# Kernel optimization log

Measured on AMD Instinct MI355X. Metric: run time of the kernel, lower is better.

## Reference

```python
import jax, jax.numpy as jnp
import numpy as np
from jax import lax

B, N, T, E = 16, 2048, 48, 32
C0, C1 = 64, 64
H1, H2 = 256, 128
NPRED = 12
KT = 3
SCALE = float(np.sqrt(C1))


def setup_inputs() -> dict:
    key = jax.random.key(0)
    ks = jax.random.split(key, 20)
    def lin(k, fin, fout):
        bound = 1.0 / np.sqrt(fin)
        kw, kb = jax.random.split(k)
        W = jax.random.uniform(kw, (fin, fout), jnp.float32, -bound, bound)
        b = jax.random.uniform(kb, (fout,), jnp.float32, -bound, bound)
        return W, b
    x = jax.random.normal(ks[0], (B, N, T, E), jnp.float32)
    W_in, b_in = lin(ks[1], E, C0)
    # conv kernel laid out WIO for lax.conv_general_dilated ('NWC','WIO','NWC')
    bound = 1.0 / np.sqrt(C0 * KT)
    W_conv = jax.random.uniform(ks[2], (KT, C0, C1), jnp.float32, -bound, bound)
    b_conv = jax.random.uniform(ks[3], (C1,), jnp.float32, -bound, bound)
    Wq, bq = lin(ks[4], C1, C1)
    Wk, bk = lin(ks[5], C1, C1)
    Wv, bv = lin(ks[6], C1, C1)
    W1, b1 = lin(ks[7], C1, H1)
    W2, b2 = lin(ks[8], H1, H2)
    W3, b3 = lin(ks[9], H2, NPRED)
    return dict(x=x, W_in=W_in, b_in=b_in, W_conv=W_conv, b_conv=b_conv,
                Wq=Wq, bq=bq, Wk=Wk, bk=bk, Wv=Wv, bv=bv,
                W1=W1, b1=b1, W2=W2, b2=b2, W3=W3, b3=b3)


def reference(x, W_in, b_in, W_conv, b_conv, Wq, bq, Wk, bk, Wv, bv,
              W1, b1, W2, b2, W3, b3):
    Bs, Ns, Ts, Es = x.shape
    # input linear, fold nodes into batch (weights shared across nodes)
    h = jnp.einsum('bnte,ec->bntc', x, W_in) + b_in          # [B,N,T,C0]
    h = h.reshape(Bs * Ns, Ts, C0)                            # [BN,T,C0]
    # temporal conv over T, kernel KT, pad 1 each side (matches Conv2d (Kt,1), pad (1,0))
    h = lax.conv_general_dilated(h, W_conv, window_strides=(1,),
                                 padding=[(1, 1)],
                                 dimension_numbers=('NWC', 'WIO', 'NWC')) + b_conv
    h = jax.nn.relu(h)                                        # [BN,T,C1]
    q = h @ Wq + bq
    k = h @ Wk + bk
    v = h @ Wv + bv
    scores = jnp.einsum('btd,bsd->bts', q, k) / SCALE         # [BN,T,T]
    attn = jax.nn.softmax(scores, axis=-1)
    ctx = jnp.einsum('bts,bsd->btd', attn, v)                 # [BN,T,C1]
    last = ctx[:, -1, :]                                      # [BN,C1]
    # output MLP (dropout is identity in eval/reference)
    z = jax.nn.relu(last @ W1 + b1)
    z = jax.nn.relu(z @ W2 + b2)
    pred = z @ W3 + b3                                        # [BN,NPRED]
    out = pred.reshape(Bs, Ns, NPRED)                         # [B,N,P]
    out = jnp.transpose(out, (0, 2, 1))[:, None]              # [B,1,P,N]
    return out
```

## Files before the change

kernel.cpp:

```cpp
#include <hip/hip_runtime.h>
#include <math.h>

#define TT 48
#define NSEQ (16*2048)
#define NP 12

typedef __bf16 bf16x8 __attribute__((ext_vector_type(8)));
typedef float  f32x4  __attribute__((ext_vector_type(4)));

#define OFF_WCC 0
#define OFF_WK  6144
#define OFF_WV  10240
#define OFF_WQ  14336
#define OFF_W1  18432
#define OFF_W2  34816
#define WS_BTOT 33792
#define WS_BC0  33856
#define WS_BC2  33920
#define WS_CTX  33984

__device__ __forceinline__ f32x4 zero4() {
  f32x4 z; z[0] = 0.f; z[1] = 0.f; z[2] = 0.f; z[3] = 0.f; return z;
}

__global__ __launch_bounds__(256) void prep_kernel(
    const float* __restrict__ W_in, const float* __restrict__ b_in,
    const float* __restrict__ W_conv, const float* __restrict__ b_conv,
    const float* __restrict__ Wk, const float* __restrict__ Wv,
    const float* __restrict__ Wq, const float* __restrict__ W1,
    const float* __restrict__ W2, float* __restrict__ ws)
{
  __bf16* wsb = (__bf16*)ws;
  const int tid = threadIdx.x;
  const int bid = blockIdx.x;
  if (bid < 24) {
    int gid = bid * 256 + tid;
    int kk = gid >> 6;
    int c  = gid & 63;
    int dt = kk >> 5;
    int e  = kk & 31;
    const float* wrow = W_in + e * 64;
    const float* wc   = W_conv + dt * 4096 + c;
    float acc = 0.f;
    #pragma unroll 8
    for (int c0 = 0; c0 < 64; ++c0)
      acc = fmaf(wrow[c0], wc[c0 * 64], acc);
    wsb[OFF_WCC + ((kk >> 3) * 64 + c) * 8 + (kk & 7)] = (__bf16)acc;
  } else if (bid < 40) {
    int gid = (bid - 24) * 256 + tid;
    int kk = gid >> 6, c = gid & 63;
    wsb[OFF_WK + ((kk >> 3) * 64 + c) * 8 + (kk & 7)] = (__bf16)Wk[kk * 64 + c];
  } else if (bid < 56) {
    int gid = (bid - 40) * 256 + tid;
    int kk = gid >> 6, c = gid & 63;
    wsb[OFF_WV + ((kk >> 3) * 64 + c) * 8 + (kk & 7)] = (__bf16)Wv[kk * 64 + c];
  } else if (bid < 72) {
    int gid = (bid - 56) * 256 + tid;
    int kk = gid >> 6, c = gid & 63;
    wsb[OFF_WQ + ((kk >> 3) * 64 + c) * 8 + (kk & 7)] = (__bf16)Wq[kk * 64 + c];
  } else if (bid < 136) {
    int gid = (bid - 72) * 256 + tid;
    int kk = gid >> 8, n = gid & 255;
    wsb[OFF_W1 + ((kk >> 3) * 256 + n) * 8 + (kk & 7)] = (__bf16)W1[kk * 256 + n];
  } else if (bid < 264) {
    int gid = (bid - 136) * 256 + tid;
    int kk = gid >> 7, n = gid & 127;
    wsb[OFF_W2 + ((kk >> 3) * 128 + n) * 8 + (kk & 7)] = (__bf16)W2[kk * 128 + n];
  } else if (tid < 64) {
    int c = tid;
    float s[3];
    for (int dt = 0; dt < 3; ++dt) {
      const float* wc = W_conv + dt * 4096 + c;
      float a = 0.f;
      for (int c0 = 0; c0 < 64; ++c0) a = fmaf(b_in[c0], wc[c0 * 64], a);
      s[dt] = a;
    }
    ws[WS_BC0 + c]  = s[0];
    ws[WS_BC2 + c]  = s[2];
    ws[WS_BTOT + c] = s[0] + s[1] + s[2] + b_conv[c];
  }
}

__global__ __launch_bounds__(256, 2) void attn_kernel(
    const float* __restrict__ x,
    const float* __restrict__ bq, const float* __restrict__ bk,
    const float* __restrict__ bv,
    const float* __restrict__ ws, float* __restrict__ ctx)
{
  __shared__ __bf16 h1s[4][48 * 66];

  const int tid  = threadIdx.x;
  const int lane = tid & 63;
  const int wv   = tid >> 6;
  const int m16  = lane & 15;
  const int quad = lane >> 4;
  const int seq  = blockIdx.x * 4 + wv;
  __bf16* h1 = h1s[wv];

  const __bf16* wsb  = (const __bf16*)ws;
  const bf16x8* WccB = (const bf16x8*)(wsb + OFF_WCC);
  const bf16x8* WkB  = (const bf16x8*)(wsb + OFF_WK);
  const bf16x8* WvB  = (const bf16x8*)(wsb + OFF_WV);
  const bf16x8* WqB  = (const bf16x8*)(wsb + OFF_WQ);
  const float*  wsf  = ws;
  const float*  xseq = x + (size_t)seq * (TT * 32);

  f32x4 cacc[3][4];
  #pragma unroll
  for (int mt = 0; mt < 3; ++mt)
    #pragma unroll
    for (int nt = 0; nt < 4; ++nt) cacc[mt][nt] = zero4();

  #pragma unroll
  for (int ks = 0; ks < 3; ++ks) {
    bf16x8 bf[4];
    #pragma unroll
    for (int nt = 0; nt < 4; ++nt)
      bf[nt] = WccB[(ks * 4 + quad) * 64 + nt * 16 + m16];
    #pragma unroll
    for (int mt = 0; mt < 3; ++mt) {
      const int tg = mt * 16 + m16 + ks - 1;
      const bool need_guard = (mt == 0 && ks == 0) || (mt == 2 && ks == 2);
      bf16x8 af;
      if (!need_guard || (tg >= 0 && tg < 48)) {
        const float* ap = xseq + tg * 32 + quad * 8;
        float4 a0 = *(const float4*)ap;
        float4 a1 = *(const float4*)(ap + 4);
        af[0] = (__bf16)a0.x; af[1] = (__bf16)a0.y;
        af[2] = (__bf16)a0.z; af[3] = (__bf16)a0.w;
        af[4] = (__bf16)a1.x; af[5] = (__bf16)a1.y;
        af[6] = (__bf16)a1.z; af[7] = (__bf16)a1.w;
      } else {
        #pragma unroll
        for (int j = 0; j < 8; ++j) af[j] = (__bf16)0.f;
      }
      #pragma unroll
      for (int nt = 0; nt < 4; ++nt)
        cacc[mt][nt] = __builtin_amdgcn_mfma_f32_16x16x32_bf16(af, bf[nt], cacc[mt][nt], 0, 0, 0);
    }
  }

  #pragma unroll
  for (int nt = 0; nt < 4; ++nt) {
    const int c = nt * 16 + m16;
    const float bt = wsf[WS_BTOT + c];
    const float b0 = wsf[WS_BC0 + c];
    const float b2 = wsf[WS_BC2 + c];
    #pragma unroll
    for (int mt = 0; mt < 3; ++mt)
      #pragma unroll
      for (int r = 0; r < 4; ++r) {
        const int trow = mt * 16 + quad * 4 + r;
        float v = cacc[mt][nt][r] + bt;
        if (mt == 0 && r == 0 && quad == 0) v -= b0;
        if (mt == 2 && r == 3 && quad == 3) v -= b2;
        h1[trow * 66 + c] = (__bf16)fmaxf(v, 0.f);
      }
  }
  __asm__ __volatile__("s_waitcnt lgkmcnt(0)" ::: "memory");

  bf16x8 a8[3][2];
  #pragma unroll
  for (int mt = 0; mt < 3; ++mt)
    #pragma unroll
    for (int ks = 0; ks < 2; ++ks)
      a8[mt][ks] = *(const bf16x8*)&h1[(mt * 16 + m16) * 66 + ks * 32 + quad * 8];

  float qvv[4];
  {
    f32x4 qa[4] = {zero4(), zero4(), zero4(), zero4()};
    #pragma unroll
    for (int ks = 0; ks < 2; ++ks)
      #pragma unroll
      for (int nt = 0; nt < 4; ++nt)
        qa[nt] = __builtin_amdgcn_mfma_f32_16x16x32_bf16(
            a8[2][ks], WqB[(ks * 4 + quad) * 64 + nt * 16 + m16], qa[nt], 0, 0, 0);
    #pragma unroll
    for (int nt = 0; nt < 4; ++nt) {
      float q47 = __shfl(qa[nt][3], m16 + 48, 64);
      qvv[nt] = (q47 + bq[nt * 16 + m16]) * 0.125f;
    }
  }

  float p[3][4];
  {
    f32x4 ka[3][4];
    #pragma unroll
    for (int mt = 0; mt < 3; ++mt)
      #pragma unroll
      for (int nt = 0; nt < 4; ++nt) ka[mt][nt] = zero4();
    #pragma unroll
    for (int ks = 0; ks < 2; ++ks) {
      bf16x8 bf[4];
      #pragma unroll
      for (int nt = 0; nt < 4; ++nt)
        bf[nt] = WkB[(ks * 4 + quad) * 64 + nt * 16 + m16];
      #pragma unroll
      for (int mt = 0; mt < 3; ++mt)
        #pragma unroll
        for (int nt = 0; nt < 4; ++nt)
          ka[mt][nt] = __builtin_amdgcn_mfma_f32_16x16x32_bf16(a8[mt][ks], bf[nt], ka[mt][nt], 0, 0, 0);
    }
    float qb = 0.f;
    #pragma unroll
    for (int nt = 0; nt < 4; ++nt) qb = fmaf(qvv[nt], bk[nt * 16 + m16], qb);
    float s[3][4];
    #pragma unroll
    for (int mt = 0; mt < 3; ++mt)
      #pragma unroll
      for (int r = 0; r < 4; ++r) {
        float t = qb;
        #pragma unroll
        for (int nt = 0; nt < 4; ++nt) t = fmaf(qvv[nt], ka[mt][nt][r], t);
        t += __shfl_xor(t, 1, 64);
        t += __shfl_xor(t, 2, 64);
        t += __shfl_xor(t, 4, 64);
        t += __shfl_xor(t, 8, 64);
        s[mt][r] = t;
      }
    float mx = -INFINITY;
    #pragma unroll
    for (int mt = 0; mt < 3; ++mt)
      #pragma unroll
      for (int r = 0; r < 4; ++r) mx = fmaxf(mx, s[mt][r]);
    mx = fmaxf(mx, __shfl_xor(mx, 16, 64));
    mx = fmaxf(mx, __shfl_xor(mx, 32, 64));
    float l = 0.f;
    #pragma unroll
    for (int mt = 0; mt < 3; ++mt)
      #pragma unroll
      for (int r = 0; r < 4; ++r) {
        float e = __expf(s[mt][r] - mx);
        p[mt][r] = e;
        l += e;
      }
    l += __shfl_xor(l, 16, 64);
    l += __shfl_xor(l, 32, 64);
    float rl = 1.f / l;
    #pragma unroll
    for (int mt = 0; mt < 3; ++mt)
      #pragma unroll
      for (int r = 0; r < 4; ++r) p[mt][r] *= rl;
  }

  {
    f32x4 va[3][4];
    #pragma unroll
    for (int mt = 0; mt < 3; ++mt)
      #pragma unroll
      for (int nt = 0; nt < 4; ++nt) va[mt][nt] = zero4();
    #pragma unroll
    for (int ks = 0; ks < 2; ++ks) {
      bf16x8 bf[4];
      #pragma unroll
      for (int nt = 0; nt < 4; ++nt)
        bf[nt] = WvB[(ks * 4 + quad) * 64 + nt * 16 + m16];
      #pragma unroll
      for (int mt = 0; mt < 3; ++mt)
        #pragma unroll
        for (int nt = 0; nt < 4; ++nt)
          va[mt][nt] = __builtin_amdgcn_mfma_f32_16x16x32_bf16(a8[mt][ks], bf[nt], va[mt][nt], 0, 0, 0);
    }
    float cx[4] = {0.f, 0.f, 0.f, 0.f};
    #pragma unroll
    for (int nt = 0; nt < 4; ++nt)
      #pragma unroll
      for (int mt = 0; mt < 3; ++mt)
        #pragma unroll
        for (int r = 0; r < 4; ++r)
          cx[nt] = fmaf(p[mt][r], va[mt][nt][r], cx[nt]);
    #pragma unroll
    for (int nt = 0; nt < 4; ++nt) {
      cx[nt] += __shfl_xor(cx[nt], 16, 64);
      cx[nt] += __shfl_xor(cx[nt], 32, 64);
    }
    if (quad == 0) {
      #pragma unroll
      for (int nt = 0; nt < 4; ++nt)
        ctx[(size_t)seq * 64 + nt * 16 + m16] = cx[nt] + bv[nt * 16 + m16];
    }
  }
}

__global__ __launch_bounds__(256) void mlp_kernel(
    const float* __restrict__ ctx, const float* __restrict__ ws,
    const float* __restrict__ b1, const float* __restrict__ b2,
    const float* __restrict__ W3, const float* __restrict__ b3,
    float* __restrict__ out)
{
  __shared__ __bf16 Xs[16 * 68];
  __shared__ __bf16 z1[16 * 264];
  __shared__ float  z2[16 * 132];

  const int tid  = threadIdx.x;
  const int r0   = blockIdx.x * 16;
  const int lane = tid & 63;
  const int wv   = tid >> 6;
  const int m16  = lane & 15;
  const int quad = lane >> 4;

  const __bf16* wsb = (const __bf16*)ws;
  const bf16x8* W1B = (const bf16x8*)(wsb + OFF_W1);
  const bf16x8* W2B = (const bf16x8*)(wsb + OFF_W2);

  {
    int row = tid >> 4, c4 = (tid & 15) * 4;
    float4 a = *(const float4*)(ctx + (size_t)(r0 + row) * 64 + c4);
    __bf16* d = &Xs[row * 68 + c4];
    d[0] = (__bf16)a.x; d[1] = (__bf16)a.y; d[2] = (__bf16)a.z; d[3] = (__bf16)a.w;
  }
  __syncthreads();

  {
    bf16x8 a8[2];
    #pragma unroll
    for (int ks = 0; ks < 2; ++ks)
      a8[ks] = *(const bf16x8*)&Xs[m16 * 68 + ks * 32 + quad * 8];
    f32x4 acc[4] = {zero4(), zero4(), zero4(), zero4()};
    #pragma unroll
    for (int nt = 0; nt < 4; ++nt) {
      int n = wv * 64 + nt * 16 + m16;
      #pragma unroll
      for (int ks = 0; ks < 2; ++ks)
        acc[nt] = __builtin_amdgcn_mfma_f32_16x16x32_bf16(
            a8[ks], W1B[(ks * 4 + quad) * 256 + n], acc[nt], 0, 0, 0);
    }
    #pragma unroll
    for (int nt = 0; nt < 4; ++nt) {
      int n = wv * 64 + nt * 16 + m16;
      float bb = b1[n];
      #pragma unroll
      for (int r = 0; r < 4; ++r)
        z1[(quad * 4 + r) * 264 + n] = (__bf16)fmaxf(acc[nt][r] + bb, 0.f);
    }
  }
  __syncthreads();

  {
    f32x4 acc[2] = {zero4(), zero4()};
    #pragma unroll 2
    for (int ks = 0; ks < 8; ++ks) {
      bf16x8 a = *(const bf16x8*)&z1[m16 * 264 + ks * 32 + quad * 8];
      #pragma unroll
      for (int nt = 0; nt < 2; ++nt)
        acc[nt] = __builtin_amdgcn_mfma_f32_16x16x32_bf16(
            a, W2B[(ks * 4 + quad) * 128 + wv * 32 + nt * 16 + m16], acc[nt], 0, 0, 0);
    }
    #pragma unroll
    for (int nt = 0; nt < 2; ++nt) {
      int n = wv * 32 + nt * 16 + m16;
      float bb = b2[n];
      #pragma unroll
      for (int r = 0; r < 4; ++r)
        z2[(quad * 4 + r) * 132 + n] = fmaxf(acc[nt][r] + bb, 0.f);
    }
  }
  __syncthreads();

  if (tid < 16 * NP) {
    int r = tid / NP, pp = tid - r * NP;
    const float* zr = z2 + r * 132;
    float a0 = b3[pp], a1 = 0.f, a2 = 0.f, a3 = 0.f;
    #pragma unroll 8
    for (int k = 0; k < 128; k += 4) {
      float4 f = *(const float4*)(zr + k);
      a0 = fmaf(f.x, W3[k * NP + pp],       a0);
      a1 = fmaf(f.y, W3[(k + 1) * NP + pp], a1);
      a2 = fmaf(f.z, W3[(k + 2) * NP + pp], a2);
      a3 = fmaf(f.w, W3[(k + 3) * NP + pp], a3);
    }
    float a = (a0 + a1) + (a2 + a3);
    int row = r0 + r;
    int bb = row >> 11, nn = row & 2047;
    out[(size_t)bb * (NP * 2048) + pp * 2048 + nn] = a;
  }
}

extern "C" void kernel_launch(void* const* d_in, const int* in_sizes, int n_in,
                              void* d_out, int out_size, void* d_ws, size_t ws_size,
                              hipStream_t stream) {
  const float* x      = (const float*)d_in[0];
  const float* W_in   = (const float*)d_in[1];
  const float* b_in   = (const float*)d_in[2];
  const float* W_conv = (const float*)d_in[3];
  const float* b_conv = (const float*)d_in[4];
  const float* Wq     = (const float*)d_in[5];
  const float* bq     = (const float*)d_in[6];
  const float* Wk     = (const float*)d_in[7];
  const float* bk     = (const float*)d_in[8];
  const float* Wv     = (const float*)d_in[9];
  const float* bv     = (const float*)d_in[10];
  const float* W1     = (const float*)d_in[11];
  const float* b1     = (const float*)d_in[12];
  const float* W2     = (const float*)d_in[13];
  const float* b2     = (const float*)d_in[14];
  const float* W3     = (const float*)d_in[15];
  const float* b3     = (const float*)d_in[16];
  float* ws  = (float*)d_ws;
  float* out = (float*)d_out;

  prep_kernel<<<265, 256, 0, stream>>>(W_in, b_in, W_conv, b_conv, Wk, Wv, Wq, W1, W2, ws);
  attn_kernel<<<NSEQ / 4, 256, 0, stream>>>(x, bq, bk, bv, ws, ws + WS_CTX);
  mlp_kernel<<<NSEQ / 16, 256, 0, stream>>>(ws + WS_CTX, ws, b1, b2, W3, b3, out);
}
```

Before: 399.1 us.

## Split attention MFMA accumulators into column halves and shrink blocks for occupancy

The attention kernel now computes the conv, K and V projections in two 32-column halves, so only 6 accumulator tiles are live at once instead of 12. The conv input fragments are loaded into registers up front, and the fp32-to-bf16 conversion uses packed bf162 conversions. Blocks drop to 128 threads (2 waves, 2 sequences each) with launch bounds of 4 blocks per CU, aiming for lower register pressure and higher occupancy. The cost is reloading weight fragments per half and holding 9 preloaded input fragments, which could offset the register savings.

```diff
diff --git a/kernel.cpp b/kernel.cpp
--- a/kernel.cpp
+++ b/kernel.cpp
@@ -1,4 +1,5 @@
 #include <hip/hip_runtime.h>
+#include <hip/hip_bf16.h>
 #include <math.h>
 
 #define TT 48
@@ -21,6 +22,17 @@
 
 __device__ __forceinline__ f32x4 zero4() {
   f32x4 z; z[0] = 0.f; z[1] = 0.f; z[2] = 0.f; z[3] = 0.f; return z;
+}
+
+union PackU { bf16x8 v; __hip_bfloat162 h[4]; };
+
+__device__ __forceinline__ bf16x8 pack8(float4 a, float4 b) {
+  PackU u;
+  u.h[0] = __float22bfloat162_rn(make_float2(a.x, a.y));
+  u.h[1] = __float22bfloat162_rn(make_float2(a.z, a.w));
+  u.h[2] = __float22bfloat162_rn(make_float2(b.x, b.y));
+  u.h[3] = __float22bfloat162_rn(make_float2(b.z, b.w));
+  return u.v;
 }
 
 __global__ __launch_bounds__(256) void prep_kernel(
@@ -81,20 +93,20 @@
   }
 }
 
-__global__ __launch_bounds__(256, 2) void attn_kernel(
+__global__ __launch_bounds__(128, 4) void attn_kernel(
     const float* __restrict__ x,
     const float* __restrict__ bq, const float* __restrict__ bk,
     const float* __restrict__ bv,
     const float* __restrict__ ws, float* __restrict__ ctx)
 {
-  __shared__ __bf16 h1s[4][48 * 66];
+  __shared__ __bf16 h1s[2][48 * 66];
 
   const int tid  = threadIdx.x;
   const int lane = tid & 63;
   const int wv   = tid >> 6;
   const int m16  = lane & 15;
   const int quad = lane >> 4;
-  const int seq  = blockIdx.x * 4 + wv;
+  const int seq  = blockIdx.x * 2 + wv;
   __bf16* h1 = h1s[wv];
 
   const __bf16* wsb  = (const __bf16*)ws;
@@ -105,57 +117,54 @@
   const float*  wsf  = ws;
   const float*  xseq = x + (size_t)seq * (TT * 32);
 
-  f32x4 cacc[3][4];
+  bf16x8 af[3][3];
   #pragma unroll
   for (int mt = 0; mt < 3; ++mt)
     #pragma unroll
-    for (int nt = 0; nt < 4; ++nt) cacc[mt][nt] = zero4();
-
-  #pragma unroll
-  for (int ks = 0; ks < 3; ++ks) {
-    bf16x8 bf[4];
-    #pragma unroll
-    for (int nt = 0; nt < 4; ++nt)
-      bf[nt] = WccB[(ks * 4 + quad) * 64 + nt * 16 + m16];
-    #pragma unroll
-    for (int mt = 0; mt < 3; ++mt) {
+    for (int ks = 0; ks < 3; ++ks) {
       const int tg = mt * 16 + m16 + ks - 1;
       const bool need_guard = (mt == 0 && ks == 0) || (mt == 2 && ks == 2);
-      bf16x8 af;
       if (!need_guard || (tg >= 0 && tg < 48)) {
         const float* ap = xseq + tg * 32 + quad * 8;
-        float4 a0 = *(const float4*)ap;
-        float4 a1 = *(const float4*)(ap + 4);
-        af[0] = (__bf16)a0.x; af[1] = (__bf16)a0.y;
-        af[2] = (__bf16)a0.z; af[3] = (__bf16)a0.w;
-        af[4] = (__bf16)a1.x; af[5] = (__bf16)a1.y;
-        af[6] = (__bf16)a1.z; af[7] = (__bf16)a1.w;
+        af[mt][ks] = pack8(*(const float4*)ap, *(const float4*)(ap + 4));
       } else {
         #pragma unroll
-        for (int j = 0; j < 8; ++j) af[j] = (__bf16)0.f;
-      }
-      #pragma unroll
-      for (int nt = 0; nt < 4; ++nt)
-        cacc[mt][nt] = __builtin_amdgcn_mfma_f32_16x16x32_bf16(af, bf[nt], cacc[mt][nt], 0, 0, 0);
-    }
-  }
+        for (int j = 0; j < 8; ++j) af[mt][ks][j] = (__bf16)0.f;
+      }
+    }
 
   #pragma unroll
-  for (int nt = 0; nt < 4; ++nt) {
-    const int c = nt * 16 + m16;
-    const float bt = wsf[WS_BTOT + c];
-    const float b0 = wsf[WS_BC0 + c];
-    const float b2 = wsf[WS_BC2 + c];
-    #pragma unroll
-    for (int mt = 0; mt < 3; ++mt)
-      #pragma unroll
-      for (int r = 0; r < 4; ++r) {
-        const int trow = mt * 16 + quad * 4 + r;
-        float v = cacc[mt][nt][r] + bt;
-        if (mt == 0 && r == 0 && quad == 0) v -= b0;
-        if (mt == 2 && r == 3 && quad == 3) v -= b2;
-        h1[trow * 66 + c] = (__bf16)fmaxf(v, 0.f);
-      }
+  for (int nh = 0; nh < 2; ++nh) {
+    f32x4 acc[3][2];
+    #pragma unroll
+    for (int mt = 0; mt < 3; ++mt) { acc[mt][0] = zero4(); acc[mt][1] = zero4(); }
+    #pragma unroll
+    for (int ks = 0; ks < 3; ++ks) {
+      bf16x8 b0 = WccB[(ks * 4 + quad) * 64 + nh * 32 + m16];
+      bf16x8 b1 = WccB[(ks * 4 + quad) * 64 + nh * 32 + 16 + m16];
+      #pragma unroll
+      for (int mt = 0; mt < 3; ++mt) {
+        acc[mt][0] = __builtin_amdgcn_mfma_f32_16x16x32_bf16(af[mt][ks], b0, acc[mt][0], 0, 0, 0);
+        acc[mt][1] = __builtin_amdgcn_mfma_f32_16x16x32_bf16(af[mt][ks], b1, acc[mt][1], 0, 0, 0);
+      }
+    }
+    #pragma unroll
+    for (int j = 0; j < 2; ++j) {
+      const int c = nh * 32 + j * 16 + m16;
+      const float bt = wsf[WS_BTOT + c];
+      const float b0v = wsf[WS_BC0 + c];
+      const float b2v = wsf[WS_BC2 + c];
+      #pragma unroll
+      for (int mt = 0; mt < 3; ++mt)
+        #pragma unroll
+        for (int r = 0; r < 4; ++r) {
+          const int trow = mt * 16 + quad * 4 + r;
+          float v = acc[mt][j][r] + bt;
+          if (mt == 0 && r == 0 && quad == 0) v -= b0v;
+          if (mt == 2 && r == 3 && quad == 3) v -= b2v;
+          h1[trow * 66 + c] = (__bf16)fmaxf(v, 0.f);
+        }
+    }
   }
   __asm__ __volatile__("s_waitcnt lgkmcnt(0)" ::: "memory");
 
@@ -184,34 +193,44 @@
 
   float p[3][4];
   {
-    f32x4 ka[3][4];
+    float s[3][4];
+    {
+      float qb = 0.f;
+      #pragma unroll
+      for (int nt = 0; nt < 4; ++nt) qb = fmaf(qvv[nt], bk[nt * 16 + m16], qb);
+      #pragma unroll
+      for (int mt = 0; mt < 3; ++mt)
+        #pragma unroll
+        for (int r = 0; r < 4; ++r) s[mt][r] = qb;
+    }
+    #pragma unroll
+    for (int nh = 0; nh < 2; ++nh) {
+      f32x4 ka[3][2];
+      #pragma unroll
+      for (int mt = 0; mt < 3; ++mt) { ka[mt][0] = zero4(); ka[mt][1] = zero4(); }
+      #pragma unroll
+      for (int ks = 0; ks < 2; ++ks) {
+        bf16x8 b0 = WkB[(ks * 4 + quad) * 64 + nh * 32 + m16];
+        bf16x8 b1 = WkB[(ks * 4 + quad) * 64 + nh * 32 + 16 + m16];
+        #pragma unroll
+        for (int mt = 0; mt < 3; ++mt) {
+          ka[mt][0] = __builtin_amdgcn_mfma_f32_16x16x32_bf16(a8[mt][ks], b0, ka[mt][0], 0, 0, 0);
+          ka[mt][1] = __builtin_amdgcn_mfma_f32_16x16x32_bf16(a8[mt][ks], b1, ka[mt][1], 0, 0, 0);
+        }
+      }
+      #pragma unroll
+      for (int mt = 0; mt < 3; ++mt)
+        #pragma unroll
+        for (int r = 0; r < 4; ++r) {
+          s[mt][r] = fmaf(qvv[nh * 2],     ka[mt][0][r], s[mt][r]);
+          s[mt][r] = fmaf(qvv[nh * 2 + 1], ka[mt][1][r], s[mt][r]);
+        }
+    }
     #pragma unroll
     for (int mt = 0; mt < 3; ++mt)
       #pragma unroll
-      for (int nt = 0; nt < 4; ++nt) ka[mt][nt] = zero4();
-    #pragma unroll
-    for (int ks = 0; ks < 2; ++ks) {
-      bf16x8 bf[4];
-      #pragma unroll
-      for (int nt = 0; nt < 4; ++nt)
-        bf[nt] = WkB[(ks * 4 + quad) * 64 + nt * 16 + m16];
-      #pragma unroll
-      for (int mt = 0; mt < 3; ++mt)
-        #pragma unroll
-        for (int nt = 0; nt < 4; ++nt)
-          ka[mt][nt] = __builtin_amdgcn_mfma_f32_16x16x32_bf16(a8[mt][ks], bf[nt], ka[mt][nt], 0, 0, 0);
-    }
-    float qb = 0.f;
-    #pragma unroll
-    for (int nt = 0; nt < 4; ++nt) qb = fmaf(qvv[nt], bk[nt * 16 + m16], qb);
-    float s[3][4];
-    #pragma unroll
-    for (int mt = 0; mt < 3; ++mt)
-      #pragma unroll
       for (int r = 0; r < 4; ++r) {
-        float t = qb;
-        #pragma unroll
-        for (int nt = 0; nt < 4; ++nt) t = fmaf(qvv[nt], ka[mt][nt][r], t);
+        float t = s[mt][r];
         t += __shfl_xor(t, 1, 64);
         t += __shfl_xor(t, 2, 64);
         t += __shfl_xor(t, 4, 64);
@@ -244,31 +263,33 @@
   }
 
   {
-    f32x4 va[3][4];
-    #pragma unroll
-    for (int mt = 0; mt < 3; ++mt)
-      #pragma unroll
-      for (int nt = 0; nt < 4; ++nt) va[mt][nt] = zero4();
-    #pragma unroll
-    for (int ks = 0; ks < 2; ++ks) {
-      bf16x8 bf[4];
-      #pragma unroll
-      for (int nt = 0; nt < 4; ++nt)
-        bf[nt] = WvB[(ks * 4 + quad) * 64 + nt * 16 + m16];
-      #pragma unroll
-      for (int mt = 0; mt < 3; ++mt)
-        #pragma unroll
-        for (int nt = 0; nt < 4; ++nt)
-          va[mt][nt] = __builtin_amdgcn_mfma_f32_16x16x32_bf16(a8[mt][ks], bf[nt], va[mt][nt], 0, 0, 0);
-    }
-    float cx[4] = {0.f, 0.f, 0.f, 0.f};
-    #pragma unroll
-    for (int nt = 0; nt < 4; ++nt)
-      #pragma unroll
-      for (int mt = 0; mt < 3; ++mt)
-        #pragma unroll
-        for (int r = 0; r < 4; ++r)
-          cx[nt] = fmaf(p[mt][r], va[mt][nt][r], cx[nt]);
+    float cx[4];
+    #pragma unroll
+    for (int nh = 0; nh < 2; ++nh) {
+      f32x4 va[3][2];
+      #pragma unroll
+      for (int mt = 0; mt < 3; ++mt) { va[mt][0] = zero4(); va[mt][1] = zero4(); }
+      #pragma unroll
+      for (int ks = 0; ks < 2; ++ks) {
+        bf16x8 b0 = WvB[(ks * 4 + quad) * 64 + nh * 32 + m16];
+        bf16x8 b1 = WvB[(ks * 4 + quad) * 64 + nh * 32 + 16 + m16];
+        #pragma unroll
+        for (int mt = 0; mt < 3; ++mt) {
+          va[mt][0] = __builtin_amdgcn_mfma_f32_16x16x32_bf16(a8[mt][ks], b0, va[mt][0], 0, 0, 0);
+          va[mt][1] = __builtin_amdgcn_mfma_f32_16x16x32_bf16(a8[mt][ks], b1, va[mt][1], 0, 0, 0);
+        }
+      }
+      #pragma unroll
+      for (int j = 0; j < 2; ++j) {
+        float a = 0.f;
+        #pragma unroll
+        for (int mt = 0; mt < 3; ++mt)
+          #pragma unroll
+          for (int r = 0; r < 4; ++r)
+            a = fmaf(p[mt][r], va[mt][j][r], a);
+        cx[nh * 2 + j] = a;
+      }
+    }
     #pragma unroll
     for (int nt = 0; nt < 4; ++nt) {
       cx[nt] += __shfl_xor(cx[nt], 16, 64);
@@ -400,6 +421,6 @@
   float* out = (float*)d_out;
 
   prep_kernel<<<265, 256, 0, stream>>>(W_in, b_in, W_conv, b_conv, Wk, Wv, Wq, W1, W2, ws);
-  attn_kernel<<<NSEQ / 4, 256, 0, stream>>>(x, bq, bk, bv, ws, ws + WS_CTX);
+  attn_kernel<<<NSEQ / 2, 128, 0, stream>>>(x, bq, bk, bv, ws, ws + WS_CTX);
   mlp_kernel<<<NSEQ / 16, 256, 0, stream>>>(ws + WS_CTX, ws, b1, b2, W3, b3, out);
 }
```

Result: faster. 389.0 us (-2.5%).
